# Kernel optimization log

Hardware: AMD Instinct MI355X
Metric: run time of the kernel (lower is better)

Reference implementation:

```python
import jax, jax.numpy as jnp
import numpy as np
import math


def setup_inputs() -> dict:
    key = jax.random.key(0)
    k1, k2 = jax.random.split(key)
    q = jax.random.normal(k1, (2, 8, 2048, 64), dtype=jnp.float32)
    v = jax.random.normal(k2, (2, 8, 2048, 64), dtype=jnp.float32)
    return {"q": q, "v": v}


def reference(q, v):
    # q, v: [B, H, L, D]. Softmax-free Gaussian-kernel attention.
    # squared L2 distance via expanded form: ||qi||^2 + ||qj||^2 - 2 qi.qj
    # (same math as the original's broadcasted difference, without the
    #  O(B,H,L,L,D) intermediate)
    d = q.shape[-1]
    sq = jnp.sum(q * q, axis=-1)                      # [B, H, L]
    dots = jnp.einsum('bhid,bhjd->bhij', q, q)        # [B, H, L, L]
    sq_l2 = sq[..., :, None] + sq[..., None, :] - 2.0 * dots
    score = jnp.exp(-1.0 / (2.0 * math.sqrt(d)) * sq_l2)  # [B, H, L, L]
    return jnp.einsum('bhij,bhjd->bhid', score, v)    # [B, H, L, D]
```

## Files before the change

### kernel.cpp

```cpp
#include <hip/hip_runtime.h>
#include <hip/hip_bf16.h>
#include <stdint.h>

typedef __bf16 bf16_t;
typedef bf16_t bf16x8 __attribute__((ext_vector_type(8)));
typedef float f32x16 __attribute__((ext_vector_type(16)));
typedef float fvec4 __attribute__((ext_vector_type(4)));
typedef unsigned int u32x4v __attribute__((ext_vector_type(4)));

#define LEN 2048
#define DIM 64
#define NH  16

#define C_L8  0.18033688011112043f
#define C_L16 0.09016844005556021f

__device__ __forceinline__ float fexp2(float x) {
#if __has_builtin(__builtin_amdgcn_exp2f)
  return __builtin_amdgcn_exp2f(x);
#else
  return exp2f(x);
#endif
}

__device__ __forceinline__ unsigned pk2(float lo, float hi) {
  union { bf16_t h; unsigned short u; } a, b;
  a.h = (bf16_t)lo; b.h = (bf16_t)hi;
  return (unsigned)a.u | ((unsigned)b.u << 16);
}

__device__ __forceinline__ void glds16(const void* g, void* l) {
  __builtin_amdgcn_global_load_lds(
      (const __attribute__((address_space(1))) void*)g,
      (__attribute__((address_space(3))) void*)l, 16, 0, 0);
}

__device__ __forceinline__ int swk(int row, int b) {
  return row * 128 + (b ^ ((row & 7) << 4));
}
__device__ __forceinline__ int swv(int row, int b) {
  return row * 256 + (b ^ ((row & 7) << 4));
}

__global__ __launch_bounds__(256) void prepass(
    const float* __restrict__ q, const float* __restrict__ v,
    bf16_t* __restrict__ kb, bf16_t* __restrict__ vt, float* __restrict__ sqw) {
  __shared__ float wlds[64];
  const int b = blockIdx.x;
  const int h = b >> 5, jb = b & 31;
  const int t = threadIdx.x;
  const float* qh = q + ((size_t)h * LEN + jb * 64) * DIM;
  const float* vh = v + ((size_t)h * LEN + jb * 64) * DIM;

  {
    const int j = t >> 2, d0 = (t & 3) * 16;
    const float* qp = qh + j * DIM + d0;
    float s = 0.f;
    bf16x8 o0, o1;
#pragma unroll
    for (int e = 0; e < 8; ++e) {
      bf16_t hh = (bf16_t)qp[e]; o0[e] = hh; float f = (float)hh; s += f * f;
    }
#pragma unroll
    for (int e = 0; e < 8; ++e) {
      bf16_t hh = (bf16_t)qp[8 + e]; o1[e] = hh; float f = (float)hh; s += f * f;
    }
    bf16_t* kp = kb + ((size_t)h * LEN + jb * 64 + j) * DIM + d0;
    *(bf16x8*)kp = o0;
    *(bf16x8*)(kp + 8) = o1;
    s += __shfl_xor(s, 1);
    s += __shfl_xor(s, 2);
    if ((t & 3) == 0) {
      wlds[j] = fexp2(-s * C_L16);
      sqw[h * LEN + jb * 64 + j] = s * C_L16;
    }
  }
  __syncthreads();
  {
    const int d = t & 63, jg = t >> 6;
    float vv[16];
#pragma unroll
    for (int e = 0; e < 16; ++e) vv[e] = vh[(jg * 16 + e) * DIM + d];
    bf16x8 o0, o1;
#pragma unroll
    for (int e = 0; e < 8; ++e)  o0[e] = (bf16_t)(vv[e] * wlds[jg * 16 + e]);
#pragma unroll
    for (int e = 0; e < 8; ++e)  o1[e] = (bf16_t)(vv[8 + e] * wlds[jg * 16 + 8 + e]);
    bf16_t* vp = vt + ((size_t)h * DIM + d) * LEN + jb * 64 + jg * 16;
    *(bf16x8*)vp = o0;
    *(bf16x8*)(vp + 8) = o1;
  }
}

__global__ __launch_bounds__(512, 4) void soft_attn_main(
    const bf16_t* __restrict__ kb, const bf16_t* __restrict__ vt,
    const float* __restrict__ sqw, float* __restrict__ out) {
  __shared__ __align__(16) char smem[65536];

  const int tid  = threadIdx.x;
  const int lane = tid & 63;
  const int wave = tid >> 6;
  const int rg   = wave & 1;
  const int par  = wave >> 1;
  const int g    = lane >> 5;
  const int nn   = lane & 31;

  const int b  = blockIdx.x;
  const int wg = ((b & 7) << 6) | (b >> 3);
  const int bh = wg >> 5;
  const int qb = wg & 31;

  const bf16_t* kh  = kb + (size_t)bh * LEN * DIM;
  const bf16_t* vth = vt + (size_t)bh * DIM * LEN;

  const int qrow = qb * 64 + rg * 32 + nn;
  bf16x8 qf[4];
  {
    const bf16_t* qp = kh + (size_t)qrow * DIM;
#pragma unroll
    for (int kc = 0; kc < 4; ++kc)
      qf[kc] = *(const bf16x8*)(qp + kc * 16 + g * 8);
  }
  const float hq = sqw[bh * LEN + qrow];

  const bf16_t* ksrc[2];
  const bf16_t* vsrc[2];
#pragma unroll
  for (int s = 0; s < 2; ++s) {
    const int krow = wave * 16 + s * 8 + (lane >> 3);
    const int kby  = ((lane & 7) * 16) ^ ((lane >> 3) << 4);
    ksrc[s] = kh + (size_t)krow * DIM + (kby >> 1);
    const int vrow = wave * 8 + s * 4 + (lane >> 4);
    const int vby  = ((lane & 15) * 16) ^ ((vrow & 7) << 4);
    vsrc[s] = vth + (size_t)vrow * LEN + (vby >> 1);
  }
  char* kdst = smem + wave * 2048;
  char* vdst = smem + 32768 + wave * 2048;

  f32x16 acc0 = {};
  f32x16 acc1 = {};

#pragma unroll
  for (int s = 0; s < 2; ++s) {
    glds16(ksrc[s], kdst + s * 1024);
    glds16(vsrc[s], vdst + s * 1024);
  }
  __syncthreads();

  int buf = 0;
  for (int it = 0; it < 16; ++it) {
    if (it + 1 < 16) {
      const int nb = buf ^ 1;
#pragma unroll
      for (int s = 0; s < 2; ++s) {
        glds16(ksrc[s] + (size_t)(it + 1) * 128 * DIM, kdst + nb * 16384 + s * 1024);
        glds16(vsrc[s] + (size_t)(it + 1) * 128,       vdst + nb * 16384 + s * 1024);
      }
    }

    const char* kb0 = smem + buf * 16384;
    const char* vb0 = smem + 32768 + buf * 16384;

    f32x16 t = {};
#pragma unroll
    for (int kc = 0; kc < 4; ++kc) {
      bf16x8 kf = *(const bf16x8*)(kb0 + swk(par * 32 + nn, kc * 32 + g * 16));
      t = __builtin_amdgcn_mfma_f32_32x32x16_bf16(kf, qf[kc], t, 0, 0, 0);
    }

    unsigned P[8];
#pragma unroll
    for (int e = 0; e < 8; ++e) {
      float s0 = fexp2(__builtin_fmaf(t[2 * e],     C_L8, -hq));
      float s1 = fexp2(__builtin_fmaf(t[2 * e + 1], C_L8, -hq));
      P[e] = pk2(s0, s1);
    }
    asm volatile("v_permlane32_swap_b32 %0, %1" : "+v"(P[0]), "+v"(P[2]));
    asm volatile("v_permlane32_swap_b32 %0, %1" : "+v"(P[1]), "+v"(P[3]));
    asm volatile("v_permlane32_swap_b32 %0, %1" : "+v"(P[4]), "+v"(P[6]));
    asm volatile("v_permlane32_swap_b32 %0, %1" : "+v"(P[5]), "+v"(P[7]));
    u32x4v f0v = { P[0], P[1], P[2], P[3] };
    u32x4v f1v = { P[4], P[5], P[6], P[7] };
    bf16x8 af0 = __builtin_bit_cast(bf16x8, f0v);
    bf16x8 af1 = __builtin_bit_cast(bf16x8, f1v);

    {
      bf16x8 v0 = *(const bf16x8*)(vb0 + swv(nn,      par * 64 + g * 16));
      bf16x8 v1 = *(const bf16x8*)(vb0 + swv(32 + nn, par * 64 + g * 16));
      acc0 = __builtin_amdgcn_mfma_f32_32x32x16_bf16(af0, v0, acc0, 0, 0, 0);
      acc1 = __builtin_amdgcn_mfma_f32_32x32x16_bf16(af0, v1, acc1, 0, 0, 0);
      v0 = *(const bf16x8*)(vb0 + swv(nn,      par * 64 + 32 + g * 16));
      v1 = *(const bf16x8*)(vb0 + swv(32 + nn, par * 64 + 32 + g * 16));
      acc0 = __builtin_amdgcn_mfma_f32_32x32x16_bf16(af1, v0, acc0, 0, 0, 0);
      acc1 = __builtin_amdgcn_mfma_f32_32x32x16_bf16(af1, v1, acc1, 0, 0, 0);
    }

    __syncthreads();
    buf ^= 1;
  }

  float* xb = (float*)smem;
  if (par != 0) {
    float* dst = xb + ((par - 1) * 2 + rg) * 2048;
#pragma unroll
    for (int r = 0; r < 16; ++r) {
      dst[r * 64 + lane]        = acc0[r];
      dst[(16 + r) * 64 + lane] = acc1[r];
    }
  }
  __syncthreads();
  if (par == 0) {
    float* op = out + ((size_t)bh * LEN + qb * 64 + rg * 32) * DIM;
#pragma unroll
    for (int r = 0; r < 16; ++r) {
      const int row = (r & 3) + 8 * (r >> 2) + 4 * g;
      float a0 = acc0[r], a1 = acc1[r];
#pragma unroll
      for (int p = 1; p < 4; ++p) {
        const float* sb = xb + ((p - 1) * 2 + rg) * 2048;
        a0 += sb[r * 64 + lane];
        a1 += sb[(16 + r) * 64 + lane];
      }
      op[(size_t)row * DIM + nn]      = a0;
      op[(size_t)row * DIM + 32 + nn] = a1;
    }
  }
}

__device__ __forceinline__ int swfb(int row, int byte) {
  return row * 128 + (byte ^ ((row & 7) << 4));
}

__global__ __launch_bounds__(512, 2) void soft_attn_fb(
    const float* __restrict__ q, const float* __restrict__ v,
    float* __restrict__ out) {
  __shared__ __align__(16) char smem[33280];
  const int tid = threadIdx.x;
  const int lane = tid & 63;
  const int wave = tid >> 6;
  const int rg = wave & 3;
  const int parity = wave >> 2;
  const int tp = tid & 255;
  const int g = lane >> 5;
  const int nn = lane & 31;
  const int wg = ((blockIdx.x & 7) << 5) | (blockIdx.x >> 3);
  const int bh = wg >> 4;
  const int qb = wg & 15;
  const float* qh = q + (size_t)bh * LEN * DIM;
  const float* vh = v + (size_t)bh * LEN * DIM;
  char* kbufp = smem + parity * 8192;
  char* vbufp = smem + 16384 + parity * 8192;
  float* wkp = (float*)(smem + 32768) + parity * 64;
  const int qrow = qb * 128 + rg * 32 + nn;
  bf16x8 qf[4];
  float sq = 0.f;
  {
    const float* qp = qh + (size_t)qrow * DIM;
#pragma unroll
    for (int kc = 0; kc < 4; ++kc) {
      const int d0 = kc * 16 + g * 8;
      fvec4 x = *(const fvec4*)(qp + d0);
      fvec4 y = *(const fvec4*)(qp + d0 + 4);
      bf16x8 t;
#pragma unroll
      for (int e = 0; e < 4; ++e) {
        bf16_t h0 = (bf16_t)x[e]; t[e] = h0; float f0 = (float)h0; sq += f0 * f0;
        bf16_t h1 = (bf16_t)y[e]; t[e + 4] = h1; float f1 = (float)h1; sq += f1 * f1;
      }
      qf[kc] = t;
    }
  }
  sq += __shfl_xor(sq, 32);
  const float hq = sq * C_L16;
  f32x16 acc0 = {};
  f32x16 acc1 = {};
  for (int it = 0; it < 16; ++it) {
    const int jt = it * 2 + parity;
    const float* kg = qh + (size_t)jt * 64 * DIM;
    const float* vg = vh + (size_t)jt * 64 * DIM;
    __syncthreads();
#pragma unroll
    for (int s = 0; s < 2; ++s) {
      const int c = tp + 256 * s;
      const int j = c >> 3;
      const int d0 = (c & 7) * 8;
      fvec4 x = *(const fvec4*)(kg + j * DIM + d0);
      fvec4 y = *(const fvec4*)(kg + j * DIM + d0 + 4);
      bf16x8 t; float p = 0.f;
#pragma unroll
      for (int e = 0; e < 4; ++e) {
        bf16_t h0 = (bf16_t)x[e]; t[e] = h0; float f0 = (float)h0; p += f0 * f0;
        bf16_t h1 = (bf16_t)y[e]; t[e + 4] = h1; float f1 = (float)h1; p += f1 * f1;
      }
      *(bf16x8*)(kbufp + swfb(j, d0 * 2)) = t;
      p += __shfl_xor(p, 1);
      p += __shfl_xor(p, 2);
      p += __shfl_xor(p, 4);
      if ((lane & 7) == 0) wkp[j] = fexp2(-p * C_L16);
    }
    __syncthreads();
    float vl[2][8];
    const int vd = tp & 63;
    const int vw = tp >> 6;
#pragma unroll
    for (int s = 0; s < 2; ++s) {
      const int j0 = vw * 8 + 32 * s;
      const float* vp = vg + j0 * DIM + vd;
#pragma unroll
      for (int r = 0; r < 8; ++r) vl[s][r] = vp[r * DIM];
    }
    bf16x8 af[4];
#pragma unroll
    for (int jsub = 0; jsub < 2; ++jsub) {
      f32x16 t = {};
#pragma unroll
      for (int kc = 0; kc < 4; ++kc) {
        bf16x8 kf = *(const bf16x8*)(kbufp + swfb(jsub * 32 + nn, kc * 32 + g * 16));
        t = __builtin_amdgcn_mfma_f32_32x32x16_bf16(kf, qf[kc], t, 0, 0, 0);
      }
      unsigned P[8];
#pragma unroll
      for (int e = 0; e < 8; ++e) {
        float s0 = fexp2(__builtin_fmaf(t[2 * e], C_L8, -hq));
        float s1 = fexp2(__builtin_fmaf(t[2 * e + 1], C_L8, -hq));
        P[e] = pk2(s0, s1);
      }
      asm volatile("v_permlane32_swap_b32 %0, %1" : "+v"(P[0]), "+v"(P[2]));
      asm volatile("v_permlane32_swap_b32 %0, %1" : "+v"(P[1]), "+v"(P[3]));
      asm volatile("v_permlane32_swap_b32 %0, %1" : "+v"(P[4]), "+v"(P[6]));
      asm volatile("v_permlane32_swap_b32 %0, %1" : "+v"(P[5]), "+v"(P[7]));
      u32x4v f0v = { P[0], P[1], P[2], P[3] };
      u32x4v f1v = { P[4], P[5], P[6], P[7] };
      af[jsub * 2] = __builtin_bit_cast(bf16x8, f0v);
      af[jsub * 2 + 1] = __builtin_bit_cast(bf16x8, f1v);
    }
#pragma unroll
    for (int s = 0; s < 2; ++s) {
      const int j0 = vw * 8 + 32 * s;
      bf16x8 t;
#pragma unroll
      for (int r = 0; r < 8; ++r) {
        float w = wkp[j0 + r];
        t[r] = (bf16_t)(vl[s][r] * w);
      }
      *(bf16x8*)(vbufp + swfb(vd, j0 * 2)) = t;
    }
    __syncthreads();
#pragma unroll
    for (int kc = 0; kc < 4; ++kc) {
      bf16x8 v0 = *(const bf16x8*)(vbufp + swfb(nn, kc * 32 + g * 16));
      bf16x8 v1 = *(const bf16x8*)(vbufp + swfb(32 + nn, kc * 32 + g * 16));
      acc0 = __builtin_amdgcn_mfma_f32_32x32x16_bf16(af[kc], v0, acc0, 0, 0, 0);
      acc1 = __builtin_amdgcn_mfma_f32_32x32x16_bf16(af[kc], v1, acc1, 0, 0, 0);
    }
  }
  __syncthreads();
  float* xb = (float*)smem + rg * 2048;
  if (parity == 1) {
#pragma unroll
    for (int r = 0; r < 16; ++r) {
      xb[r * 64 + lane] = acc0[r];
      xb[(16 + r) * 64 + lane] = acc1[r];
    }
  }
  __syncthreads();
  if (parity == 0) {
    float* op = out + ((size_t)bh * LEN + qb * 128 + rg * 32) * DIM;
#pragma unroll
    for (int r = 0; r < 16; ++r) {
      const int row = (r & 3) + 8 * (r >> 2) + 4 * g;
      op[(size_t)row * DIM + nn] = acc0[r] + xb[r * 64 + lane];
      op[(size_t)row * DIM + 32 + nn] = acc1[r] + xb[(16 + r) * 64 + lane];
    }
  }
}

extern "C" void kernel_launch(void* const* d_in, const int* in_sizes, int n_in,
                              void* d_out, int out_size, void* d_ws, size_t ws_size,
                              hipStream_t stream) {
  const float* q = (const float*)d_in[0];
  const float* v = (const float*)d_in[1];
  float* out = (float*)d_out;
  (void)in_sizes; (void)n_in; (void)out_size;

  const size_t KB_BYTES = (size_t)NH * LEN * DIM * 2;
  const size_t NEED = KB_BYTES * 2 + (size_t)NH * LEN * 4;
  if (ws_size >= NEED) {
    bf16_t* kb  = (bf16_t*)d_ws;
    bf16_t* vt  = (bf16_t*)((char*)d_ws + KB_BYTES);
    float*  sqw = (float*)((char*)d_ws + KB_BYTES * 2);
    prepass<<<dim3(512), dim3(256), 0, stream>>>(q, v, kb, vt, sqw);
    soft_attn_main<<<dim3(512), dim3(512), 0, stream>>>(kb, vt, sqw, out);
  } else {
    soft_attn_fb<<<dim3(256), dim3(512), 0, stream>>>(q, v, out);
  }
}
```

Before: 95.07 us.

## Deepen async K/V prefetch to two tiles ahead with explicit vmcnt waits

Restructures the double-buffered loop so two K/V tiles are issued before the loop and each iteration waits with a partial s_waitcnt vmcnt(4), then refills the buffer just consumed with tile it+2 after a second barrier. Loads therefore stay in flight across a whole iteration instead of being issued and fully drained within it. It also hoists all four V fragment reads ahead of the PV MFMAs and raises wave priority around the MFMA blocks. Correctness now depends on the hand-counted vmcnt value matching the number of outstanding global-to-LDS loads, and the extra barrier per iteration adds sync cost.

Result: no change. 95.56 us (+0.5%).

```diff
diff --git a/kernel.cpp b/kernel.cpp
--- a/kernel.cpp
+++ b/kernel.cpp
@@ -145,28 +145,34 @@
     glds16(ksrc[s], kdst + s * 1024);
     glds16(vsrc[s], vdst + s * 1024);
   }
-  __syncthreads();
-
-  int buf = 0;
+#pragma unroll
+  for (int s = 0; s < 2; ++s) {
+    glds16(ksrc[s] + (size_t)128 * DIM, kdst + 16384 + s * 1024);
+    glds16(vsrc[s] + (size_t)128,       vdst + 16384 + s * 1024);
+  }
+
   for (int it = 0; it < 16; ++it) {
-    if (it + 1 < 16) {
-      const int nb = buf ^ 1;
-#pragma unroll
-      for (int s = 0; s < 2; ++s) {
-        glds16(ksrc[s] + (size_t)(it + 1) * 128 * DIM, kdst + nb * 16384 + s * 1024);
-        glds16(vsrc[s] + (size_t)(it + 1) * 128,       vdst + nb * 16384 + s * 1024);
-      }
-    }
-
+    if (it < 15) {
+      asm volatile("s_waitcnt vmcnt(4)" ::: "memory");
+    } else {
+      asm volatile("s_waitcnt vmcnt(0)" ::: "memory");
+    }
+    __builtin_amdgcn_sched_barrier(0);
+    __builtin_amdgcn_s_barrier();
+    __builtin_amdgcn_sched_barrier(0);
+
+    const int buf = it & 1;
     const char* kb0 = smem + buf * 16384;
     const char* vb0 = smem + 32768 + buf * 16384;
 
     f32x16 t = {};
+    __builtin_amdgcn_s_setprio(1);
 #pragma unroll
     for (int kc = 0; kc < 4; ++kc) {
       bf16x8 kf = *(const bf16x8*)(kb0 + swk(par * 32 + nn, kc * 32 + g * 16));
       t = __builtin_amdgcn_mfma_f32_32x32x16_bf16(kf, qf[kc], t, 0, 0, 0);
     }
+    __builtin_amdgcn_s_setprio(0);
 
     unsigned P[8];
 #pragma unroll
@@ -187,16 +193,27 @@
     {
       bf16x8 v0 = *(const bf16x8*)(vb0 + swv(nn,      par * 64 + g * 16));
       bf16x8 v1 = *(const bf16x8*)(vb0 + swv(32 + nn, par * 64 + g * 16));
+      bf16x8 v2 = *(const bf16x8*)(vb0 + swv(nn,      par * 64 + 32 + g * 16));
+      bf16x8 v3 = *(const bf16x8*)(vb0 + swv(32 + nn, par * 64 + 32 + g * 16));
+      __builtin_amdgcn_s_setprio(1);
       acc0 = __builtin_amdgcn_mfma_f32_32x32x16_bf16(af0, v0, acc0, 0, 0, 0);
       acc1 = __builtin_amdgcn_mfma_f32_32x32x16_bf16(af0, v1, acc1, 0, 0, 0);
-      v0 = *(const bf16x8*)(vb0 + swv(nn,      par * 64 + 32 + g * 16));
-      v1 = *(const bf16x8*)(vb0 + swv(32 + nn, par * 64 + 32 + g * 16));
-      acc0 = __builtin_amdgcn_mfma_f32_32x32x16_bf16(af1, v0, acc0, 0, 0, 0);
-      acc1 = __builtin_amdgcn_mfma_f32_32x32x16_bf16(af1, v1, acc1, 0, 0, 0);
-    }
-
-    __syncthreads();
-    buf ^= 1;
+      acc0 = __builtin_amdgcn_mfma_f32_32x32x16_bf16(af1, v2, acc0, 0, 0, 0);
+      acc1 = __builtin_amdgcn_mfma_f32_32x32x16_bf16(af1, v3, acc1, 0, 0, 0);
+      __builtin_amdgcn_s_setprio(0);
+    }
+
+    __builtin_amdgcn_sched_barrier(0);
+    __builtin_amdgcn_s_barrier();
+    __builtin_amdgcn_sched_barrier(0);
+
+    if (it + 2 < 16) {
+#pragma unroll
+      for (int s = 0; s < 2; ++s) {
+        glds16(ksrc[s] + (size_t)(it + 2) * 128 * DIM, kdst + buf * 16384 + s * 1024);
+        glds16(vsrc[s] + (size_t)(it + 2) * 128,       vdst + buf * 16384 + s * 1024);
+      }
+    }
   }
 
   float* xb = (float*)smem;
```
